# Kernel optimization log

Hardware: AMD Instinct MI355X
Metric: run time of the kernel (lower is better)

Reference implementation:

```python
import jax, jax.numpy as jnp
import numpy as np

N_EXPERTS = 8
Z_DIM = 128
HID = 1024
OUT = 3072  # e.g. 3x32x32 flattened generator output
BATCH = 2048


def hash_vectors(z, n):
    """Deterministic per-sample hash -> expert index in [0, n).

    Proxy for the repo's hash_vectors (which hashes the latent vector):
    quantize |z|, sum over feature dim, mod n. Non-differentiable by design.
    """
    return jnp.mod(jnp.floor(jnp.abs(z) * 1000.0).sum(axis=1).astype(jnp.int32), n)


def setup_inputs() -> dict:
    key = jax.random.key(0)
    kz, k1, kb1, k2, kb2 = jax.random.split(key, 5)
    z = jax.random.normal(kz, (BATCH, Z_DIM), dtype=jnp.float32)
    s1 = 1.0 / np.sqrt(Z_DIM)
    s2 = 1.0 / np.sqrt(HID)
    # Stacked per-expert MLP params (each expert independently initialized,
    # mirroring reset_parameters on each deepcopy).
    W1 = jax.random.uniform(k1, (N_EXPERTS, Z_DIM, HID), jnp.float32, -s1, s1)
    b1 = jax.random.uniform(kb1, (N_EXPERTS, HID), jnp.float32, -s1, s1)
    W2 = jax.random.uniform(k2, (N_EXPERTS, HID, OUT), jnp.float32, -s2, s2)
    b2 = jax.random.uniform(kb2, (N_EXPERTS, OUT), jnp.float32, -s2, s2)
    return {"z": z, "W1": W1, "b1": b1, "W2": W2, "b2": b2}


def reference(z, W1, b1, W2, b2):
    # Hard routing: each sample i goes to expert idx[i].
    idx = hash_vectors(z, N_EXPERTS)  # [B]
    # Dense compute-all-experts then select (vectorized replacement for the
    # per-sample Python loop in the original forward).
    h = jax.nn.relu(jnp.einsum('bi,eih->beh', z, W1) + b1[None, :, :])  # [B,E,H]
    y = jnp.einsum('beh,eho->beo', h, W2) + b2[None, :, :]              # [B,E,O]
    out = jnp.take_along_axis(y, idx[:, None, None], axis=1)[:, 0, :]   # [B,O]
    return out
```

## Files before the change

### kernel.cpp

```cpp
#include <hip/hip_runtime.h>
#include <hip/hip_bf16.h>


#define BATCH 2048
#define ZD 128
#define HID 1024
#define OUTD 3072
#define NEXP 8

#define TMG 128
#define TNG 128
#define BKG 64
#define MAXTF 24

typedef short bf16x8 __attribute__((ext_vector_type(8)));
typedef float f32x4 __attribute__((ext_vector_type(4)));


__global__ __launch_bounds__(256) void route_kernel(const float* __restrict__ z,
                                                    __hip_bfloat16* __restrict__ zb,
                                                    int* counts, int* bucket) {
    __shared__ int lcnt[NEXP];
    __shared__ int gbase[NEXP];
    int t = threadIdx.x;
    if (t < NEXP) lcnt[t] = 0;
    __syncthreads();

    int s = blockIdx.x * 32 + (t >> 3);
    int li = t & 7;
    const float* zp = z + (size_t)s * ZD + li * 16;
    float sum = 0.f;
    union { bf16x8 v8; __hip_bfloat16 h[8]; } u0, u1;
#pragma unroll
    for (int i = 0; i < 4; i++) {
        float4 v = ((const float4*)zp)[i];
        sum += floorf(fabsf(v.x) * 1000.0f) + floorf(fabsf(v.y) * 1000.0f) +
               floorf(fabsf(v.z) * 1000.0f) + floorf(fabsf(v.w) * 1000.0f);
        __hip_bfloat16* dst = (i < 2) ? &u0.h[i * 4] : &u1.h[(i - 2) * 4];
        dst[0] = __float2bfloat16(v.x);
        dst[1] = __float2bfloat16(v.y);
        dst[2] = __float2bfloat16(v.z);
        dst[3] = __float2bfloat16(v.w);
    }
    bf16x8* zo = (bf16x8*)(zb + (size_t)s * ZD + li * 16);
    zo[0] = u0.v8;
    zo[1] = u1.v8;

    sum += __shfl_down(sum, 4);
    sum += __shfl_down(sum, 2);
    sum += __shfl_down(sum, 1);
    int e = 0, lpos = 0;
    if (li == 0) {
        e = ((int)sum) & 7;
        lpos = atomicAdd(&lcnt[e], 1);
    }
    __syncthreads();
    if (t < NEXP) gbase[t] = atomicAdd(&counts[t], lcnt[t]);
    __syncthreads();
    if (li == 0) bucket[e * BATCH + gbase[e] + lpos] = s;
}

__global__ void scan_kernel(const int* __restrict__ counts, int* ntl,
                            int* texp, int* perm, const int* __restrict__ bucket) {
    __shared__ int soff[NEXP + 1];
    __shared__ int scnt[NEXP];
    if (threadIdx.x == 0) {
        int o = 0;
        for (int e = 0; e < NEXP; e++) {
            scnt[e] = counts[e];
            soff[e] = o;
            o += (scnt[e] + TMG - 1) & ~(TMG - 1);
        }
        soff[NEXP] = o;
        *ntl = o / TMG;
    }
    __syncthreads();
    int total = soff[NEXP];
    for (int r = threadIdx.x; r < total; r += blockDim.x) {
        int e = 0;
        while (r >= soff[e + 1]) e++;
        int i = r - soff[e];
        perm[r] = (i < scnt[e]) ? bucket[e * BATCH + i] : -1;
        if ((r & (TMG - 1)) == 0) texp[r / TMG] = e;
    }
}

__global__ __launch_bounds__(256) void trans_kernel(const float* __restrict__ W,
                                                    __hip_bfloat16* __restrict__ WT,
                                                    int K, int N) {
    int e = blockIdx.z;
    int n0 = blockIdx.x * 64;
    int k0 = blockIdx.y * 128;
    const float* Wp = W + (size_t)e * K * N;
    __hip_bfloat16* Op = WT + (size_t)e * N * K;
    __shared__ __align__(16) __hip_bfloat16 Ts[64 * 16 * 8];

    int t = threadIdx.x;
    int nn = (t & 15) * 4;
    int kb = (t >> 4) * 8;
    int c = t >> 4;

    float4 v[8];
#pragma unroll
    for (int i = 0; i < 8; i++)
        v[i] = *(const float4*)(Wp + (size_t)(k0 + kb + i) * N + n0 + nn);

#pragma unroll
    for (int j = 0; j < 4; j++) {
        union { bf16x8 v8; __hip_bfloat16 h[8]; } u;
        float* f = (float*)v;
#pragma unroll
        for (int i = 0; i < 8; i++) u.h[i] = __float2bfloat16(f[i * 4 + j]);
        int n = nn + j;
        *(bf16x8*)(Ts + ((size_t)n * 16 + (c ^ (n & 7))) * 8) = u.v8;
    }
    __syncthreads();

    int n = t >> 2;
#pragma unroll
    for (int p = 0; p < 4; p++) {
        int cd = p * 4 + (t & 3);
        bf16x8 val = *(const bf16x8*)(Ts + ((size_t)n * 16 + (cd ^ (n & 7))) * 8);
        *(bf16x8*)(Op + (size_t)(n0 + n) * K + k0 + cd * 8) = val;
    }
}


__global__ __launch_bounds__(256, 3) void gemm1_fast(
    const __hip_bfloat16* __restrict__ zb, const __hip_bfloat16* __restrict__ W1T,
    const float* __restrict__ b1, const int* __restrict__ ntl,
    const int* __restrict__ texp, const int* __restrict__ perm,
    __hip_bfloat16* __restrict__ H) {
    int mt = blockIdx.y;
    if (mt >= *ntl) return;
    int e = texp[mt];
    int n0 = blockIdx.x * TNG;

    __shared__ __align__(16) __hip_bfloat16 As[TMG * BKG];
    __shared__ __align__(16) __hip_bfloat16 Bs[TNG * BKG];
    __shared__ int rows_s[TMG];

    int tid = threadIdx.x;
    if (tid < TMG) rows_s[tid] = perm[mt * TMG + tid];
    __syncthreads();

    int lane = tid & 63, wave = tid >> 6;
    int cc = lane & 15, q = lane >> 4;
    int mw = (wave >> 1) * 64, nw = (wave & 1) * 64;

    int sr = tid >> 3, sc = tid & 7;
    int wbase = sr * 64 + (sc ^ (sr & 7)) * 8;
    const __hip_bfloat16* Bg = W1T + ((size_t)e * HID + n0 + sr) * ZD + sc * 8;
    const __hip_bfloat16* Arp[4];
#pragma unroll
    for (int p = 0; p < 4; p++) {
        int r = rows_s[p * 32 + sr];
        if (r < 0) r = 0;
        Arp[p] = zb + (size_t)r * ZD + sc * 8;
    }

    int A0 = (mw + cc) * 64, B0 = (nw + cc) * 64;
    int X0 = (q ^ (cc & 7)) * 8, X1 = ((4 + q) ^ (cc & 7)) * 8;

    float bias[4];
#pragma unroll
    for (int j = 0; j < 4; j++) bias[j] = b1[(size_t)e * HID + n0 + nw + j * 16 + cc];

    f32x4 zero4 = {0.f, 0.f, 0.f, 0.f};
    f32x4 acc[4][4];
#pragma unroll
    for (int i = 0; i < 4; i++)
#pragma unroll
        for (int j = 0; j < 4; j++) acc[i][j] = zero4;

    bf16x8 ga[4], gb[4];
#pragma unroll
    for (int p = 0; p < 4; p++) {
        ga[p] = *(const bf16x8*)(Arp[p]);
        gb[p] = *(const bf16x8*)(Bg + (size_t)p * 32 * ZD);
    }
#pragma unroll
    for (int it = 0; it < ZD / BKG; ++it) {
        __syncthreads();
#pragma unroll
        for (int p = 0; p < 4; p++) {
            *(bf16x8*)(As + wbase + p * 2048) = ga[p];
            *(bf16x8*)(Bs + wbase + p * 2048) = gb[p];
        }
        __syncthreads();
        if (it + 1 < ZD / BKG) {
#pragma unroll
            for (int p = 0; p < 4; p++) {
                ga[p] = *(const bf16x8*)(Arp[p] + (it + 1) * BKG);
                gb[p] = *(const bf16x8*)(Bg + (size_t)p * 32 * ZD + (it + 1) * BKG);
            }
        }
#pragma unroll
        for (int kh = 0; kh < 2; ++kh) {
            int X = kh ? X1 : X0;
            bf16x8 af[4], bfr[4];
#pragma unroll
            for (int i = 0; i < 4; i++) af[i] = *(const bf16x8*)(As + A0 + i * 1024 + X);
#pragma unroll
            for (int j = 0; j < 4; j++) bfr[j] = *(const bf16x8*)(Bs + B0 + j * 1024 + X);
#pragma unroll
            for (int i = 0; i < 4; i++)
#pragma unroll
                for (int j = 0; j < 4; j++)
                    acc[i][j] = __builtin_amdgcn_mfma_f32_16x16x32_bf16(af[i], bfr[j],
                                                                        acc[i][j], 0, 0, 0);
        }
    }
#pragma unroll
    for (int i = 0; i < 4; i++)
#pragma unroll
        for (int r = 0; r < 4; r++) {
            int m = mw + i * 16 + q * 4 + r;
            __hip_bfloat16* hp = H + (size_t)(mt * TMG + m) * HID + n0 + nw + cc;
#pragma unroll
            for (int j = 0; j < 4; j++)
                hp[j * 16] = __float2bfloat16(fmaxf(acc[i][j][r] + bias[j], 0.f));
        }
}

__global__ __launch_bounds__(256, 3) void gemm2_fast(
    const __hip_bfloat16* __restrict__ H, const __hip_bfloat16* __restrict__ W2T,
    const float* __restrict__ b2, const int* __restrict__ ntl,
    const int* __restrict__ texp, const int* __restrict__ perm,
    float* __restrict__ out) {
    int mt = blockIdx.y;
    if (mt >= *ntl) return;
    int e = texp[mt];
    int n0 = blockIdx.x * TNG;

    __shared__ __align__(16) __hip_bfloat16 As[TMG * BKG];
    __shared__ __align__(16) __hip_bfloat16 Bs[TNG * BKG];
    __shared__ int rows_s[TMG];

    int tid = threadIdx.x;
    if (tid < TMG) rows_s[tid] = perm[mt * TMG + tid];

    int lane = tid & 63, wave = tid >> 6;
    int cc = lane & 15, q = lane >> 4;
    int mw = (wave >> 1) * 64, nw = (wave & 1) * 64;

    int sr = tid >> 3, sc = tid & 7;
    int wbase = sr * 64 + (sc ^ (sr & 7)) * 8;
    const __hip_bfloat16* Ag = H + ((size_t)mt * TMG + sr) * HID + sc * 8;
    const __hip_bfloat16* Bg = W2T + ((size_t)e * OUTD + n0 + sr) * HID + sc * 8;

    int A0 = (mw + cc) * 64, B0 = (nw + cc) * 64;
    int X0 = (q ^ (cc & 7)) * 8, X1 = ((4 + q) ^ (cc & 7)) * 8;

    float bias[4];
#pragma unroll
    for (int j = 0; j < 4; j++) bias[j] = b2[(size_t)e * OUTD + n0 + nw + j * 16 + cc];

    f32x4 zero4 = {0.f, 0.f, 0.f, 0.f};
    f32x4 acc[4][4];
#pragma unroll
    for (int i = 0; i < 4; i++)
#pragma unroll
        for (int j = 0; j < 4; j++) acc[i][j] = zero4;

    bf16x8 ga[4], gb[4];
#pragma unroll
    for (int p = 0; p < 4; p++) {
        ga[p] = *(const bf16x8*)(Ag + (size_t)p * 32 * HID);
        gb[p] = *(const bf16x8*)(Bg + (size_t)p * 32 * HID);
    }
    for (int it = 0; it < HID / BKG; ++it) {
        __syncthreads();
#pragma unroll
        for (int p = 0; p < 4; p++) {
            *(bf16x8*)(As + wbase + p * 2048) = ga[p];
            *(bf16x8*)(Bs + wbase + p * 2048) = gb[p];
        }
        __syncthreads();
        if (it + 1 < HID / BKG) {
            int k1 = (it + 1) * BKG;
#pragma unroll
            for (int p = 0; p < 4; p++) {
                ga[p] = *(const bf16x8*)(Ag + (size_t)p * 32 * HID + k1);
                gb[p] = *(const bf16x8*)(Bg + (size_t)p * 32 * HID + k1);
            }
        }
#pragma unroll
        for (int kh = 0; kh < 2; ++kh) {
            int X = kh ? X1 : X0;
            bf16x8 af[4], bfr[4];
#pragma unroll
            for (int i = 0; i < 4; i++) af[i] = *(const bf16x8*)(As + A0 + i * 1024 + X);
#pragma unroll
            for (int j = 0; j < 4; j++) bfr[j] = *(const bf16x8*)(Bs + B0 + j * 1024 + X);
#pragma unroll
            for (int i = 0; i < 4; i++)
#pragma unroll
                for (int j = 0; j < 4; j++)
                    acc[i][j] = __builtin_amdgcn_mfma_f32_16x16x32_bf16(af[i], bfr[j],
                                                                        acc[i][j], 0, 0, 0);
        }
    }
#pragma unroll
    for (int i = 0; i < 4; i++)
#pragma unroll
        for (int r = 0; r < 4; r++) {
            int m = mw + i * 16 + q * 4 + r;
            int orow = rows_s[m];
            if (orow >= 0) {
                float* op = out + (size_t)orow * OUTD + n0 + nw + cc;
#pragma unroll
                for (int j = 0; j < 4; j++) op[j * 16] = acc[i][j][r] + bias[j];
            }
        }
}

extern "C" void kernel_launch(void* const* d_in, const int* in_sizes, int n_in,
                              void* d_out, int out_size, void* d_ws, size_t ws_size,
                              hipStream_t stream) {
    const float* z  = (const float*)d_in[0];
    const float* W1 = (const float*)d_in[1];
    const float* b1 = (const float*)d_in[2];
    const float* W2 = (const float*)d_in[3];
    const float* b2 = (const float*)d_in[4];
    float* out = (float*)d_out;

    char* ws = (char*)d_ws;
    int* counts = (int*)ws;
    int* ntl    = (int*)(ws + 64);
    int* texp   = (int*)(ws + 128);
    int* perm   = (int*)(ws + 256);
    int* bucket = (int*)(ws + 12544);
    __hip_bfloat16* zb  = (__hip_bfloat16*)(ws + 78080);
    __hip_bfloat16* Hb  = (__hip_bfloat16*)(ws + 602368);
    __hip_bfloat16* W1T = (__hip_bfloat16*)(ws + 6893824);
    __hip_bfloat16* W2T = (__hip_bfloat16*)(ws + 8990976);

    hipMemsetAsync(counts, 0, 64, stream);
    hipLaunchKernelGGL(route_kernel, dim3(BATCH / 32), dim3(256), 0, stream,
                       z, zb, counts, bucket);
    hipLaunchKernelGGL(scan_kernel, dim3(1), dim3(256), 0, stream,
                       counts, ntl, texp, perm, bucket);
    hipLaunchKernelGGL(trans_kernel, dim3(HID / 64, ZD / 128, NEXP), dim3(256), 0,
                       stream, W1, W1T, ZD, HID);
    hipLaunchKernelGGL(trans_kernel, dim3(OUTD / 64, HID / 128, NEXP), dim3(256), 0,
                       stream, W2, W2T, HID, OUTD);
    hipLaunchKernelGGL(gemm1_fast, dim3(HID / TNG, MAXTF), dim3(256), 0, stream,
                       zb, W1T, b1, ntl, texp, perm, Hb);
    hipLaunchKernelGGL(gemm2_fast, dim3(OUTD / TNG, MAXTF), dim3(256), 0, stream,
                       Hb, W2T, b2, ntl, texp, perm, out);
}
```

Baseline: 215.3 us.

## Fuse weight transpose and bf16 conversion into GEMM B-tile loads

Drops the separate transpose kernels that turned fp32 W1/W2 into transposed bf16 copies. Each GEMM now reads fp32 weights straight from global memory, converts them to bf16 in registers and writes them transposed into swizzled shared memory. This removes two launches and a full write and re-read of the converted weights. In exchange, each GEMM block reads fp32 weights, twice the bytes of bf16, and every M-tile of the same expert re-reads and re-converts the same weight tile, which adds global traffic and ALU work inside the main loop.

```diff
diff --git a/kernel.cpp b/kernel.cpp
--- a/kernel.cpp
+++ b/kernel.cpp
@@ -85,49 +85,9 @@
     }
 }
 
-__global__ __launch_bounds__(256) void trans_kernel(const float* __restrict__ W,
-                                                    __hip_bfloat16* __restrict__ WT,
-                                                    int K, int N) {
-    int e = blockIdx.z;
-    int n0 = blockIdx.x * 64;
-    int k0 = blockIdx.y * 128;
-    const float* Wp = W + (size_t)e * K * N;
-    __hip_bfloat16* Op = WT + (size_t)e * N * K;
-    __shared__ __align__(16) __hip_bfloat16 Ts[64 * 16 * 8];
-
-    int t = threadIdx.x;
-    int nn = (t & 15) * 4;
-    int kb = (t >> 4) * 8;
-    int c = t >> 4;
-
-    float4 v[8];
-#pragma unroll
-    for (int i = 0; i < 8; i++)
-        v[i] = *(const float4*)(Wp + (size_t)(k0 + kb + i) * N + n0 + nn);
-
-#pragma unroll
-    for (int j = 0; j < 4; j++) {
-        union { bf16x8 v8; __hip_bfloat16 h[8]; } u;
-        float* f = (float*)v;
-#pragma unroll
-        for (int i = 0; i < 8; i++) u.h[i] = __float2bfloat16(f[i * 4 + j]);
-        int n = nn + j;
-        *(bf16x8*)(Ts + ((size_t)n * 16 + (c ^ (n & 7))) * 8) = u.v8;
-    }
-    __syncthreads();
-
-    int n = t >> 2;
-#pragma unroll
-    for (int p = 0; p < 4; p++) {
-        int cd = p * 4 + (t & 3);
-        bf16x8 val = *(const bf16x8*)(Ts + ((size_t)n * 16 + (cd ^ (n & 7))) * 8);
-        *(bf16x8*)(Op + (size_t)(n0 + n) * K + k0 + cd * 8) = val;
-    }
-}
-
 
 __global__ __launch_bounds__(256, 3) void gemm1_fast(
-    const __hip_bfloat16* __restrict__ zb, const __hip_bfloat16* __restrict__ W1T,
+    const __hip_bfloat16* __restrict__ zb, const float* __restrict__ W1,
     const float* __restrict__ b1, const int* __restrict__ ntl,
     const int* __restrict__ texp, const int* __restrict__ perm,
     __hip_bfloat16* __restrict__ H) {
@@ -149,8 +109,7 @@
     int mw = (wave >> 1) * 64, nw = (wave & 1) * 64;
 
     int sr = tid >> 3, sc = tid & 7;
-    int wbase = sr * 64 + (sc ^ (sr & 7)) * 8;
-    const __hip_bfloat16* Bg = W1T + ((size_t)e * HID + n0 + sr) * ZD + sc * 8;
+    int awbase = sr * 64 + (sc ^ (sr & 7)) * 8;
     const __hip_bfloat16* Arp[4];
 #pragma unroll
     for (int p = 0; p < 4; p++) {
@@ -158,6 +117,12 @@
         if (r < 0) r = 0;
         Arp[p] = zb + (size_t)r * ZD + sc * 8;
     }
+    int bkc = tid & 7, bn = (tid >> 3) * 4;
+    const float* Bgf = W1 + (size_t)e * ZD * HID + (size_t)(bkc * 8) * HID + n0 + bn;
+    int bwb[4];
+#pragma unroll
+    for (int j = 0; j < 4; j++)
+        bwb[j] = (bn + j) * 64 + ((bkc ^ ((bn + j) & 7))) * 8;
 
     int A0 = (mw + cc) * 64, B0 = (nw + cc) * 64;
     int X0 = (q ^ (cc & 7)) * 8, X1 = ((4 + q) ^ (cc & 7)) * 8;
@@ -173,26 +138,37 @@
 #pragma unroll
         for (int j = 0; j < 4; j++) acc[i][j] = zero4;
 
-    bf16x8 ga[4], gb[4];
-#pragma unroll
-    for (int p = 0; p < 4; p++) {
-        ga[p] = *(const bf16x8*)(Arp[p]);
-        gb[p] = *(const bf16x8*)(Bg + (size_t)p * 32 * ZD);
+    bf16x8 ga[4];
+    union { bf16x8 v8; __hip_bfloat16 h[8]; } gb[4];
+#pragma unroll
+    for (int p = 0; p < 4; p++) ga[p] = *(const bf16x8*)(Arp[p]);
+#pragma unroll
+    for (int i = 0; i < 8; i++) {
+        float4 v = *(const float4*)(Bgf + (size_t)i * HID);
+        gb[0].h[i] = __float2bfloat16(v.x);
+        gb[1].h[i] = __float2bfloat16(v.y);
+        gb[2].h[i] = __float2bfloat16(v.z);
+        gb[3].h[i] = __float2bfloat16(v.w);
     }
 #pragma unroll
     for (int it = 0; it < ZD / BKG; ++it) {
         __syncthreads();
 #pragma unroll
-        for (int p = 0; p < 4; p++) {
-            *(bf16x8*)(As + wbase + p * 2048) = ga[p];
-            *(bf16x8*)(Bs + wbase + p * 2048) = gb[p];
-        }
+        for (int p = 0; p < 4; p++) *(bf16x8*)(As + awbase + p * 2048) = ga[p];
+#pragma unroll
+        for (int j = 0; j < 4; j++) *(bf16x8*)(Bs + bwb[j]) = gb[j].v8;
         __syncthreads();
         if (it + 1 < ZD / BKG) {
 #pragma unroll
-            for (int p = 0; p < 4; p++) {
+            for (int p = 0; p < 4; p++)
                 ga[p] = *(const bf16x8*)(Arp[p] + (it + 1) * BKG);
-                gb[p] = *(const bf16x8*)(Bg + (size_t)p * 32 * ZD + (it + 1) * BKG);
+#pragma unroll
+            for (int i = 0; i < 8; i++) {
+                float4 v = *(const float4*)(Bgf + (size_t)((it + 1) * BKG + i) * HID);
+                gb[0].h[i] = __float2bfloat16(v.x);
+                gb[1].h[i] = __float2bfloat16(v.y);
+                gb[2].h[i] = __float2bfloat16(v.z);
+                gb[3].h[i] = __float2bfloat16(v.w);
             }
         }
 #pragma unroll
@@ -224,7 +200,7 @@
 }
 
 __global__ __launch_bounds__(256, 3) void gemm2_fast(
-    const __hip_bfloat16* __restrict__ H, const __hip_bfloat16* __restrict__ W2T,
+    const __hip_bfloat16* __restrict__ H, const float* __restrict__ W2,
     const float* __restrict__ b2, const int* __restrict__ ntl,
     const int* __restrict__ texp, const int* __restrict__ perm,
     float* __restrict__ out) {
@@ -245,9 +221,14 @@
     int mw = (wave >> 1) * 64, nw = (wave & 1) * 64;
 
     int sr = tid >> 3, sc = tid & 7;
-    int wbase = sr * 64 + (sc ^ (sr & 7)) * 8;
+    int awbase = sr * 64 + (sc ^ (sr & 7)) * 8;
     const __hip_bfloat16* Ag = H + ((size_t)mt * TMG + sr) * HID + sc * 8;
-    const __hip_bfloat16* Bg = W2T + ((size_t)e * OUTD + n0 + sr) * HID + sc * 8;
+    int bkc = tid & 7, bn = (tid >> 3) * 4;
+    const float* Bgf = W2 + (size_t)e * HID * OUTD + (size_t)(bkc * 8) * OUTD + n0 + bn;
+    int bwb[4];
+#pragma unroll
+    for (int j = 0; j < 4; j++)
+        bwb[j] = (bn + j) * 64 + ((bkc ^ ((bn + j) & 7))) * 8;
 
     int A0 = (mw + cc) * 64, B0 = (nw + cc) * 64;
     int X0 = (q ^ (cc & 7)) * 8, X1 = ((4 + q) ^ (cc & 7)) * 8;
@@ -263,26 +244,37 @@
 #pragma unroll
         for (int j = 0; j < 4; j++) acc[i][j] = zero4;
 
-    bf16x8 ga[4], gb[4];
-#pragma unroll
-    for (int p = 0; p < 4; p++) {
-        ga[p] = *(const bf16x8*)(Ag + (size_t)p * 32 * HID);
-        gb[p] = *(const bf16x8*)(Bg + (size_t)p * 32 * HID);
+    bf16x8 ga[4];
+    union { bf16x8 v8; __hip_bfloat16 h[8]; } gb[4];
+#pragma unroll
+    for (int p = 0; p < 4; p++) ga[p] = *(const bf16x8*)(Ag + (size_t)p * 32 * HID);
+#pragma unroll
+    for (int i = 0; i < 8; i++) {
+        float4 v = *(const float4*)(Bgf + (size_t)i * OUTD);
+        gb[0].h[i] = __float2bfloat16(v.x);
+        gb[1].h[i] = __float2bfloat16(v.y);
+        gb[2].h[i] = __float2bfloat16(v.z);
+        gb[3].h[i] = __float2bfloat16(v.w);
     }
     for (int it = 0; it < HID / BKG; ++it) {
         __syncthreads();
 #pragma unroll
-        for (int p = 0; p < 4; p++) {
-            *(bf16x8*)(As + wbase + p * 2048) = ga[p];
-            *(bf16x8*)(Bs + wbase + p * 2048) = gb[p];
-        }
+        for (int p = 0; p < 4; p++) *(bf16x8*)(As + awbase + p * 2048) = ga[p];
+#pragma unroll
+        for (int j = 0; j < 4; j++) *(bf16x8*)(Bs + bwb[j]) = gb[j].v8;
         __syncthreads();
         if (it + 1 < HID / BKG) {
             int k1 = (it + 1) * BKG;
 #pragma unroll
-            for (int p = 0; p < 4; p++) {
+            for (int p = 0; p < 4; p++)
                 ga[p] = *(const bf16x8*)(Ag + (size_t)p * 32 * HID + k1);
-                gb[p] = *(const bf16x8*)(Bg + (size_t)p * 32 * HID + k1);
+#pragma unroll
+            for (int i = 0; i < 8; i++) {
+                float4 v = *(const float4*)(Bgf + (size_t)(k1 + i) * OUTD);
+                gb[0].h[i] = __float2bfloat16(v.x);
+                gb[1].h[i] = __float2bfloat16(v.y);
+                gb[2].h[i] = __float2bfloat16(v.z);
+                gb[3].h[i] = __float2bfloat16(v.w);
             }
         }
 #pragma unroll
@@ -333,20 +325,14 @@
     int* bucket = (int*)(ws + 12544);
     __hip_bfloat16* zb  = (__hip_bfloat16*)(ws + 78080);
     __hip_bfloat16* Hb  = (__hip_bfloat16*)(ws + 602368);
-    __hip_bfloat16* W1T = (__hip_bfloat16*)(ws + 6893824);
-    __hip_bfloat16* W2T = (__hip_bfloat16*)(ws + 8990976);
 
     hipMemsetAsync(counts, 0, 64, stream);
     hipLaunchKernelGGL(route_kernel, dim3(BATCH / 32), dim3(256), 0, stream,
                        z, zb, counts, bucket);
     hipLaunchKernelGGL(scan_kernel, dim3(1), dim3(256), 0, stream,
                        counts, ntl, texp, perm, bucket);
-    hipLaunchKernelGGL(trans_kernel, dim3(HID / 64, ZD / 128, NEXP), dim3(256), 0,
-                       stream, W1, W1T, ZD, HID);
-    hipLaunchKernelGGL(trans_kernel, dim3(OUTD / 64, HID / 128, NEXP), dim3(256), 0,
-                       stream, W2, W2T, HID, OUTD);
     hipLaunchKernelGGL(gemm1_fast, dim3(HID / TNG, MAXTF), dim3(256), 0, stream,
-                       zb, W1T, b1, ntl, texp, perm, Hb);
+                       zb, W1, b1, ntl, texp, perm, Hb);
     hipLaunchKernelGGL(gemm2_fast, dim3(OUTD / TNG, MAXTF), dim3(256), 0, stream,
-                       Hb, W2T, b2, ntl, texp, perm, out);
-}
+                       Hb, W2, b2, ntl, texp, perm, out);
+}
```

After: 218.2 us. Within noise of the previous version (+1.3%).
